# Performance work log

Measured on AMD Instinct MI355X. Metric: run time of the kernel, lower is better.

## Reference

```python
import jax, jax.numpy as jnp
import numpy as np

N_NODES = 20000
N_EDGES = 320000
EMB = 256
K_DIFF = 3
BN_EPS = 1e-5


def conv1d(x, w, b, stride):
    # x: [N, Cin, L], w: [Cout, Cin, K]
    y = jax.lax.conv_general_dilated(x, w, window_strides=(stride,), padding='VALID',
                                     dimension_numbers=('NCH', 'OIH', 'NCH'))
    return y + b[None, :, None]


def batchnorm_train(x, gamma, beta):
    # training-mode BatchNorm1d over (N, L) per channel, biased variance
    m = jnp.mean(x, axis=(0, 2), keepdims=True)
    v = jnp.var(x, axis=(0, 2), keepdims=True)
    return (x - m) * jax.lax.rsqrt(v + BN_EPS) * gamma[None, :, None] + beta[None, :, None]


def dconv(X, W, b, row, col, norm_out, norm_in, n):
    # Diffusion convolution (pytorch_geometric_temporal DConv), K hops,
    # forward (out-degree) and backward (in-degree) random walks.
    def prop(x, norm):
        msg = norm[:, None] * x[row]                    # [E, F] gather
        return jax.ops.segment_sum(msg, col, num_segments=n)  # scatter-add to targets

    K = W.shape[1]
    Tx_0 = X
    Tx_1 = X
    H = X @ W[0, 0] + X @ W[1, 0]
    if K > 1:
        Tx_1_o = prop(X, norm_out)
        Tx_1_i = prop(X, norm_in)
        H = H + Tx_1_o @ W[0, 1] + Tx_1_i @ W[1, 1]
    for k in range(2, K):
        Tx_2_o = 2.0 * prop(Tx_1_o, norm_out) - Tx_0
        Tx_2_i = 2.0 * prop(Tx_1_i, norm_in) - Tx_0
        H = H + Tx_2_o @ W[0, k] + Tx_2_i @ W[1, k]
        Tx_0, Tx_1_o, Tx_1_i = Tx_1, Tx_2_o, Tx_2_i
    return H + b


def setup_inputs() -> dict:
    key = jax.random.key(0)
    ks = jax.random.split(key, 16)
    d_in = 2 * EMB  # concat([X, H])
    inp = {
        'x': jax.random.normal(ks[0], (N_NODES, 1, 100), dtype=jnp.float32),
        'edge_index': jax.random.randint(ks[1], (2, N_EDGES), 0, N_NODES, dtype=jnp.int32),
        'hidden_state': jax.random.normal(ks[2], (N_NODES, EMB), dtype=jnp.float32),
        'conv1_w': jax.random.normal(ks[3], (32, 1, 10), dtype=jnp.float32) * 0.2,
        'conv1_b': jnp.zeros((32,), jnp.float32),
        'bn1_gamma': jnp.ones((32,), jnp.float32),
        'bn1_beta': jnp.zeros((32,), jnp.float32),
        'conv2_w': jax.random.normal(ks[4], (32, 32, 10), dtype=jnp.float32) * 0.05,
        'conv2_b': jnp.zeros((32,), jnp.float32),
        'bn2_gamma': jnp.ones((32,), jnp.float32),
        'bn2_beta': jnp.zeros((32,), jnp.float32),
        'W_z': jax.random.normal(ks[5], (2, K_DIFF, d_in, EMB), dtype=jnp.float32) * 0.05,
        'b_z': jnp.zeros((EMB,), jnp.float32),
        'W_r': jax.random.normal(ks[6], (2, K_DIFF, d_in, EMB), dtype=jnp.float32) * 0.05,
        'b_r': jnp.zeros((EMB,), jnp.float32),
        'W_h': jax.random.normal(ks[7], (2, K_DIFF, d_in, EMB), dtype=jnp.float32) * 0.05,
        'b_h': jnp.zeros((EMB,), jnp.float32),
    }
    return inp


def reference(x, edge_index, hidden_state, conv1_w, conv1_b, bn1_gamma, bn1_beta,
              conv2_w, conv2_b, bn2_gamma, bn2_beta, W_z, b_z, W_r, b_r, W_h, b_h):
    n = x.shape[0]
    # CNN embedding: conv -> relu -> bn, twice
    h = batchnorm_train(jax.nn.relu(conv1d(x, conv1_w, conv1_b, 3)), bn1_gamma, bn1_beta)
    h = batchnorm_train(jax.nn.relu(conv1d(h, conv2_w, conv2_b, 3)), bn2_gamma, bn2_beta)
    X = h.reshape(n, -1)  # [N, EMB]

    row, col = edge_index[0], edge_index[1]
    ones = jnp.ones((row.shape[0],), X.dtype)
    deg_out = jax.ops.segment_sum(ones, row, num_segments=n)
    deg_in = jax.ops.segment_sum(ones, col, num_segments=n)
    norm_out = (1.0 / deg_out)[row]
    norm_in = (1.0 / deg_in)[col]

    H0 = hidden_state
    XH = jnp.concatenate([X, H0], axis=1)
    Z = jax.nn.sigmoid(dconv(XH, W_z, b_z, row, col, norm_out, norm_in, n))
    R = jax.nn.sigmoid(dconv(XH, W_r, b_r, row, col, norm_out, norm_in, n))
    XRH = jnp.concatenate([X, R * H0], axis=1)
    H_tilde = jnp.tanh(dconv(XRH, W_h, b_h, row, col, norm_out, norm_in, n))
    H = Z * H0 + (1.0 - Z) * H_tilde
    return jax.nn.relu(H)
```

## Files before the change

### kernel.cpp

```cpp
#include <hip/hip_runtime.h>
#include <cstdint>
#include <cstddef>

#define NN 20000
#define NE 320000
#define SBUF 10240000

typedef float f32x4 __attribute__((ext_vector_type(4)));
typedef short s16x8 __attribute__((ext_vector_type(8)));
typedef unsigned short us;

__device__ __forceinline__ us f2bf(float x){
    unsigned u = __float_as_uint(x);
    unsigned r = (u + 0x7fffu + ((u >> 16) & 1u)) >> 16;
    return (us)r;
}
__device__ __forceinline__ float bf2f(us s){
    return __uint_as_float(((unsigned)s) << 16);
}

__device__ __forceinline__ void gl16(const void* g, void* l){
    __builtin_amdgcn_global_load_lds((const __attribute__((address_space(1))) unsigned int*)g,
                                     (__attribute__((address_space(3))) unsigned int*)l, 16, 0, 0);
}

__device__ __forceinline__ void upd8(uint4 v, float w, float* ao, float* ai){
    float f0=__uint_as_float(v.x<<16), f1=__uint_as_float(v.x&0xffff0000u);
    float f2=__uint_as_float(v.y<<16), f3=__uint_as_float(v.y&0xffff0000u);
    float f4=__uint_as_float(v.z<<16), f5=__uint_as_float(v.z&0xffff0000u);
    float f6=__uint_as_float(v.w<<16), f7=__uint_as_float(v.w&0xffff0000u);
    ao[0]=fmaf(w,f0,ao[0]); ao[1]=fmaf(w,f1,ao[1]); ao[2]=fmaf(w,f2,ao[2]); ao[3]=fmaf(w,f3,ao[3]);
    ao[4]=fmaf(w,f4,ao[4]); ao[5]=fmaf(w,f5,ao[5]); ao[6]=fmaf(w,f6,ao[6]); ao[7]=fmaf(w,f7,ao[7]);
    ai[0]+=f0; ai[1]+=f1; ai[2]+=f2; ai[3]+=f3; ai[4]+=f4; ai[5]+=f5; ai[6]+=f6; ai[7]+=f7;
}
__device__ __forceinline__ void updw(uint4 v, float w, float* a){
    float f0=__uint_as_float(v.x<<16), f1=__uint_as_float(v.x&0xffff0000u);
    float f2=__uint_as_float(v.y<<16), f3=__uint_as_float(v.y&0xffff0000u);
    float f4=__uint_as_float(v.z<<16), f5=__uint_as_float(v.z&0xffff0000u);
    float f6=__uint_as_float(v.w<<16), f7=__uint_as_float(v.w&0xffff0000u);
    a[0]=fmaf(w,f0,a[0]); a[1]=fmaf(w,f1,a[1]); a[2]=fmaf(w,f2,a[2]); a[3]=fmaf(w,f3,a[3]);
    a[4]=fmaf(w,f4,a[4]); a[5]=fmaf(w,f5,a[5]); a[6]=fmaf(w,f6,a[6]); a[7]=fmaf(w,f7,a[7]);
}
__device__ __forceinline__ uint4 pack8(const float* a){
    uint4 r;
    r.x=((unsigned)f2bf(a[1])<<16)|f2bf(a[0]);
    r.y=((unsigned)f2bf(a[3])<<16)|f2bf(a[2]);
    r.z=((unsigned)f2bf(a[5])<<16)|f2bf(a[4]);
    r.w=((unsigned)f2bf(a[7])<<16)|f2bf(a[6]);
    return r;
}
__device__ __forceinline__ uint4 pack8s(const float* a, float s){
    uint4 r;
    r.x=((unsigned)f2bf(s*a[1])<<16)|f2bf(s*a[0]);
    r.y=((unsigned)f2bf(s*a[3])<<16)|f2bf(s*a[2]);
    r.z=((unsigned)f2bf(s*a[5])<<16)|f2bf(s*a[4]);
    r.w=((unsigned)f2bf(s*a[7])<<16)|f2bf(s*a[6]);
    return r;
}


__global__ void k_zero(uint32_t* p, int n){
    int i = blockIdx.x*256 + threadIdx.x;
    if(i < n) p[i] = 0u;
}

__global__ void k_degree(const int* __restrict__ ei, int* degout, int* degin){
    int e = blockIdx.x*256 + threadIdx.x;
    if(e < NE){
        atomicAdd(&degout[ei[e]], 1);
        atomicAdd(&degin[ei[NE+e]], 1);
    }
}

__global__ void k_scan(const int* __restrict__ degin, int* __restrict__ coloff,
                       float* __restrict__ invdegin){
    __shared__ int part[1024];
    int t = threadIdx.x;
    int base = t*20;
    int s = 0;
    for(int k=0;k<20;k++){ int i = base+k; if(i < NN) s += degin[i]; }
    part[t] = s;
    __syncthreads();
    for(int off=1; off<1024; off<<=1){
        int v = (t>=off) ? part[t-off] : 0;
        __syncthreads();
        part[t] += v;
        __syncthreads();
    }
    int run = (t>0) ? part[t-1] : 0;
    for(int k=0;k<20;k++){
        int i = base+k;
        if(i < NN){
            int d = degin[i];
            coloff[i] = run;
            run += d;
            invdegin[i] = (d>0) ? (1.0f/(float)d) : 0.0f;
        }
    }
    if(t==1023) coloff[NN] = part[1023];
}

__global__ void k_csr(const int* __restrict__ ei, const int* __restrict__ degout,
                      const int* __restrict__ coloff, int* cnt, int2* __restrict__ ew){
    int e = blockIdx.x*256 + threadIdx.x;
    if(e < NE){
        int r = ei[e], c = ei[NE+e];
        int pos = coloff[c] + atomicAdd(&cnt[c], 1);
        int2 v; v.x = r; v.y = __float_as_int(1.0f/(float)degout[r]);
        ew[pos] = v;
    }
}


__global__ void k_conv1(const float* __restrict__ x, const float* __restrict__ w1,
                        const float* __restrict__ b1, us* __restrict__ y1T){
    __shared__ float w[320];
    __shared__ float bb[32];
    int t = threadIdx.x;
    for(int i=t;i<320;i+=256) w[i] = w1[i];
    if(t < 32) bb[t] = b1[t];
    __syncthreads();
    int gid = blockIdx.x*256 + t;
    int node = gid>>5, p = gid&31;
    us* yo = y1T + (size_t)node*1024 + p*32;
    if(p >= 31){
        uint4 z = {0,0,0,0};
        *(uint4*)yo = z; *(uint4*)(yo+8) = z;
        *(uint4*)(yo+16) = z; *(uint4*)(yo+24) = z;
        return;
    }
    const float* xr = x + node*100 + 3*p;
    float xv[10];
    #pragma unroll
    for(int k=0;k<10;k++) xv[k] = xr[k];
    float o[32];
    #pragma unroll
    for(int c=0;c<32;c++){
        float a = bb[c];
        #pragma unroll
        for(int k=0;k<10;k++) a = fmaf(w[c*10+k], xv[k], a);
        o[c] = fmaxf(a, 0.0f);
    }
    *(uint4*)yo      = pack8(o);
    *(uint4*)(yo+8)  = pack8(o+8);
    *(uint4*)(yo+16) = pack8(o+16);
    *(uint4*)(yo+24) = pack8(o+24);
}

__global__ void k_chanstats_T(const us* __restrict__ y, float* __restrict__ sq){
    int tid = blockIdx.x*256 + threadIdx.x;
    int slot = tid & 1023;
    int c = slot & 31;
    int node0 = tid >> 10;
    float s = 0.f, q = 0.f;
    for(int n=node0; n<NN; n+=64){
        float v = bf2f(y[(size_t)n*1024 + slot]);
        s += v; q = fmaf(v, v, q);
    }
    s += __shfl_xor(s, 32);
    q += __shfl_xor(q, 32);
    if((threadIdx.x & 63) < 32){
        atomicAdd(&sq[c], s);
        atomicAdd(&sq[32+c], q);
    }
}

template<int SLOTS, int PPC>
__global__ void k_chanstats_bf(const us* __restrict__ y, float* __restrict__ sq){
    int tid = blockIdx.x*blockDim.x + threadIdx.x;
    int slot = tid & (SLOTS-1);
    int node0 = tid / SLOTS;
    int nstride = (gridDim.x*blockDim.x) / SLOTS;
    int c = slot / PPC;
    float s = 0.f, q = 0.f;
    for(int n=node0; n<NN; n+=nstride){
        float v = bf2f(y[(size_t)n*SLOTS + slot]);
        s += v; q = fmaf(v, v, q);
    }
    #pragma unroll
    for(int m=PPC>>1; m>0; m>>=1){
        s += __shfl_xor(s, m);
        q += __shfl_xor(q, m);
    }
    if((threadIdx.x & (PPC-1)) == 0){
        atomicAdd(&sq[c], s);
        atomicAdd(&sq[32+c], q);
    }
}

__global__ void k_bnfin(const float* __restrict__ sq, const float* __restrict__ gamma,
                        const float* __restrict__ beta, float* __restrict__ scsh,
                        float inv_count){
    int c = threadIdx.x;
    if(c < 32){
        float m = sq[c]*inv_count;
        float v = sq[32+c]*inv_count - m*m;
        float sc = gamma[c]*rsqrtf(v + 1e-5f);
        scsh[c] = sc;
        scsh[32+c] = beta[c] - m*sc;
    }
}

__global__ void k_wfold(const float* __restrict__ w2, const float* __restrict__ scsh1,
                        us* __restrict__ Bf){
    int idx = blockIdx.x*256 + threadIdx.x;
    if(idx >= 10240) return;
    int kk = idx >> 10, c2 = (idx >> 5) & 31, c = idx & 31;
    Bf[idx] = f2bf(scsh1[c] * w2[c2*320 + c*10 + kk]);
}

__global__ void k_wbias(const float* __restrict__ w2, const float* __restrict__ scsh1,
                        const float* __restrict__ b2, float* __restrict__ biasc){
    int t = threadIdx.x;
    int c2 = t >> 3, part = t & 7;
    float s = 0.f;
    for(int i=part; i<320; i+=8)
        s += scsh1[32 + i/10] * w2[c2*320 + i];
    s += __shfl_xor(s,1); s += __shfl_xor(s,2); s += __shfl_xor(s,4);
    if(part == 0) biasc[c2] = b2[c2] + s;
}

__global__ void __launch_bounds__(256) k_conv2m(const us* __restrict__ y1T,
        const us* __restrict__ Bf, const float* __restrict__ biasc,
        us* __restrict__ Xpre){
    int t = threadIdx.x;
    int wv = t>>6, l = t&63;
    int l15 = l&15, g = l>>4;
    int r0 = blockIdx.x*64 + wv*16;
    int arow = r0 + l15;
    int an = arow>>3, ap = arow&7;
    const us* abase = y1T + (size_t)an*1024 + (3*ap)*32 + g*8;
    const us* bbase = Bf + (size_t)l15*32 + g*8;
    f32x4 acc0 = {}, acc1 = {};
    #pragma unroll
    for(int kk=0;kk<10;kk++){
        s16x8 af = *(const s16x8*)(abase + kk*32);
        s16x8 b0 = *(const s16x8*)(bbase + kk*1024);
        s16x8 b1 = *(const s16x8*)(bbase + kk*1024 + 512);
        acc0 = __builtin_amdgcn_mfma_f32_16x16x32_bf16(af, b0, acc0, 0, 0, 0);
        acc1 = __builtin_amdgcn_mfma_f32_16x16x32_bf16(af, b1, acc1, 0, 0, 0);
    }
    int base = r0 + g*4;
    int n = base>>3, p0 = base&7;
    #pragma unroll
    for(int nf=0;nf<2;nf++){
        int c2 = nf*16 + l15;
        float bb = biasc[c2];
        f32x4 a = nf ? acc1 : acc0;
        float v0 = fmaxf(a[0]+bb,0.f), v1 = fmaxf(a[1]+bb,0.f);
        float v2 = fmaxf(a[2]+bb,0.f), v3 = fmaxf(a[3]+bb,0.f);
        uint2 pk;
        pk.x = ((unsigned)f2bf(v1)<<16)|f2bf(v0);
        pk.y = ((unsigned)f2bf(v3)<<16)|f2bf(v2);
        *(uint2*)&Xpre[(size_t)n*256 + c2*8 + p0] = pk;
    }
}

__global__ void __launch_bounds__(256) k_prep(const us* __restrict__ Xpre,
        const float* __restrict__ scsh, const float* __restrict__ h0,
        us* __restrict__ XHp){
    int node = blockIdx.x*4 + (threadIdx.x>>6);
    if(node >= NN) return;
    int lane = threadIdx.x & 63;
    int half = lane>>5, g = lane&31;
    uint4 o;
    if(half == 0){
        uint4 v = *(const uint4*)(Xpre + (size_t)node*256 + g*8);
        float sc = scsh[g], sh = scsh[32+g];
        float y[8];
        y[0]=fmaf(sc,__uint_as_float(v.x<<16),sh); y[1]=fmaf(sc,__uint_as_float(v.x&0xffff0000u),sh);
        y[2]=fmaf(sc,__uint_as_float(v.y<<16),sh); y[3]=fmaf(sc,__uint_as_float(v.y&0xffff0000u),sh);
        y[4]=fmaf(sc,__uint_as_float(v.z<<16),sh); y[5]=fmaf(sc,__uint_as_float(v.z&0xffff0000u),sh);
        y[6]=fmaf(sc,__uint_as_float(v.w<<16),sh); y[7]=fmaf(sc,__uint_as_float(v.w&0xffff0000u),sh);
        o = pack8(y);
    }else{
        float4 a = *(const float4*)(h0 + (size_t)node*256 + g*8);
        float4 b = *(const float4*)(h0 + (size_t)node*256 + g*8 + 4);
        float y[8] = {a.x,a.y,a.z,a.w,b.x,b.y,b.z,b.w};
        o = pack8(y);
    }
    *(uint4*)(XHp + (size_t)node*512 + (size_t)g*16 + half*8) = o;
}


__device__ __forceinline__ float weff_val(const float* W, int term, size_t base){
    const size_t S = 512*256;
    if(term==0)      return W[0*S+base] + W[3*S+base] - W[2*S+base] - W[5*S+base];
    else if(term==1) return W[1*S+base];
    else if(term==2) return W[4*S+base];
    else if(term==3) return 2.0f*W[2*S+base];
    else             return 2.0f*W[5*S+base];
}

template<int NCOL>
__global__ void __launch_bounds__(256) k_wefft(const float* __restrict__ Wa,
        const float* __restrict__ Wb, us* __restrict__ Wt){
    __shared__ float tile[64*65];
    int bx = blockIdx.x;
    constexpr int CT = NCOL/64;
    int kb = bx / (CT*4);
    int rem = bx % (CT*4);
    int ct = rem >> 2, rt = rem & 3;
    int col0 = ct*64, rr0 = rt*64;
    const float* W = (col0 < 256) ? Wa : Wb;
    int jb = col0 & 255;
    int term = kb >> 1, half = kb & 1;
    int t = threadIdx.x;
    int j_l = t & 63, r4 = t >> 6;
    #pragma unroll
    for(int it=0; it<16; it++){
        int rr_l = it*4 + r4;
        int row = half*256 + rr0 + rr_l;
        size_t base = (size_t)row*256 + jb + j_l;
        tile[j_l*65 + rr_l] = weff_val(W, term, base);
    }
    __syncthreads();
    int rr_w = t & 63;
    #pragma unroll
    for(int it=0; it<16; it++){
        int col_l = it*4 + r4;
        Wt[(size_t)(col0+col_l)*2560 + kb*256 + rr0 + rr_w] = f2bf(tile[col_l*65 + rr_w]);
    }
}


__global__ void __launch_bounds__(256) k_prop1(const us* __restrict__ XHp,
        const int* __restrict__ coloff, const int2* __restrict__ ew,
        const float* __restrict__ invdeg, us* __restrict__ T1op, us* __restrict__ T1ip){
    int node = blockIdx.x*4 + (threadIdx.x>>6);
    if(node >= NN) return;
    int lane = threadIdx.x & 63;
    size_t lo = (size_t)(lane&31)*16 + (lane>>5)*8;
    int s = __builtin_amdgcn_readfirstlane(coloff[node]);
    int e = __builtin_amdgcn_readfirstlane(coloff[node+1]);
    float ao[8]={0,0,0,0,0,0,0,0}, ai[8]={0,0,0,0,0,0,0,0};
    int j = s;
    for(; j+7 < e; j += 8){
        int2 ed[8]; uint4 v[8];
        #pragma unroll
        for(int i=0;i<8;i++) ed[i] = ew[j+i];
        #pragma unroll
        for(int i=0;i<8;i++) v[i] = *(const uint4*)(XHp+(size_t)ed[i].x*512+lo);
        #pragma unroll
        for(int i=0;i<8;i++) upd8(v[i], __int_as_float(ed[i].y), ao, ai);
    }
    for(; j < e; j++){
        int2 ed = ew[j];
        uint4 v = *(const uint4*)(XHp+(size_t)ed.x*512+lo);
        upd8(v, __int_as_float(ed.y), ao, ai);
    }
    float wi = invdeg[node];
    *(uint4*)(T1op+(size_t)node*512+lo) = pack8(ao);
    *(uint4*)(T1ip+(size_t)node*512+lo) = pack8s(ai,wi);
}

__global__ void __launch_bounds__(256) k_prop2(const us* __restrict__ T1op,
        const us* __restrict__ T1ip,
        const int* __restrict__ coloff, const int2* __restrict__ ew,
        const float* __restrict__ invdeg, us* __restrict__ P2op, us* __restrict__ P2ip){
    int node = blockIdx.x*4 + (threadIdx.x>>6);
    if(node >= NN) return;
    int lane = threadIdx.x & 63;
    size_t lo = (size_t)(lane&31)*16 + (lane>>5)*8;
    int s = __builtin_amdgcn_readfirstlane(coloff[node]);
    int e = __builtin_amdgcn_readfirstlane(coloff[node+1]);
    float ao[8]={0,0,0,0,0,0,0,0}, ai[8]={0,0,0,0,0,0,0,0};
    int j = s;
    for(; j+3 < e; j += 4){
        int2 ed[4]; uint4 va[4], vb[4];
        #pragma unroll
        for(int i=0;i<4;i++) ed[i] = ew[j+i];
        #pragma unroll
        for(int i=0;i<4;i++){
            size_t o = (size_t)ed[i].x*512+lo;
            va[i] = *(const uint4*)(T1op+o);
            vb[i] = *(const uint4*)(T1ip+o);
        }
        #pragma unroll
        for(int i=0;i<4;i++){
            updw(va[i], __int_as_float(ed[i].y), ao);
            updw(vb[i], 1.0f, ai);
        }
    }
    for(; j < e; j++){
        int2 ed = ew[j];
        size_t o = (size_t)ed.x*512+lo;
        updw(*(const uint4*)(T1op+o), __int_as_float(ed.y), ao);
        updw(*(const uint4*)(T1ip+o), 1.0f, ai);
    }
    float wi = invdeg[node];
    *(uint4*)(P2op+(size_t)node*512+lo) = pack8(ao);
    *(uint4*)(P2ip+(size_t)node*512+lo) = pack8s(ai,wi);
}

__global__ void __launch_bounds__(256) k_propu(const us* __restrict__ Yin,
        const int* __restrict__ coloff, const int2* __restrict__ ew,
        const float* __restrict__ invdeg, us* __restrict__ Pout){
    int node = blockIdx.x*4 + (threadIdx.x>>6);
    if(node >= NN) return;
    int lane = threadIdx.x & 63;
    int half = lane>>5;
    size_t lo = (size_t)(lane&31)*16 + half*8;
    int s = __builtin_amdgcn_readfirstlane(coloff[node]);
    int e = __builtin_amdgcn_readfirstlane(coloff[node+1]);
    float a[8]={0,0,0,0,0,0,0,0};
    int j = s;
    for(; j+7 < e; j += 8){
        int2 ed[8]; uint4 v[8];
        #pragma unroll
        for(int i=0;i<8;i++) ed[i] = ew[j+i];
        #pragma unroll
        for(int i=0;i<8;i++) v[i] = *(const uint4*)(Yin+(size_t)ed[i].x*512+lo);
        #pragma unroll
        for(int i=0;i<8;i++) updw(v[i], half ? 1.0f : __int_as_float(ed[i].y), a);
    }
    for(; j < e; j++){
        int2 ed = ew[j];
        uint4 v = *(const uint4*)(Yin+(size_t)ed.x*512+lo);
        updw(v, half ? 1.0f : __int_as_float(ed.y), a);
    }
    float sc = half ? invdeg[node] : 1.0f;
    *(uint4*)(Pout+(size_t)node*512+lo) = pack8s(a,sc);
}


template<int MODE, int BNT>
__global__ void __launch_bounds__(256) k_gemm(const us* __restrict__ XG,
        const us* __restrict__ RG, const us* __restrict__ Wt,
        const float* __restrict__ bias0, const float* __restrict__ bias1,
        const float* __restrict__ h0, const float* __restrict__ Zin,
        float* __restrict__ out0, us* __restrict__ out1){
    constexpr int WN = BNT/32;
    constexpr int NB = BNT/64;
    __shared__ us As[3][4096];
    __shared__ us Bs[3][BNT*32];
    int t = threadIdx.x;
    int wid = t >> 6, lane = t & 63;
    int l15 = lane & 15, kg = lane >> 4;

    int bid = blockIdx.x;
    int xcd = bid & 7, sblk = bid >> 3;
    int cidx = sblk & 3, r = (sblk >> 2)*8 + xcd;
    if(r >= 157) return;
    int row0 = r*128, col0 = cidx*BNT;
    int rowbase = (wid >> 1)*64, colbase = (wid & 1)*(BNT/2);
    int swz = (l15 >> 1) & 3;

    int srA[2], sgA[2];
    size_t rowoffA[2];
    #pragma unroll
    for(int i=0;i<2;i++){
        int c = t + i*256;
        srA[i] = c >> 2;
        sgA[i] = (c & 3) ^ ((srA[i] >> 1) & 3);
        int gr = row0 + srA[i];
        gr = (gr < NN) ? gr : NN-1;
        rowoffA[i] = (size_t)gr*512 + (size_t)sgA[i]*16;
    }
    int srB[NB], sgB[NB];
    size_t coloffB[NB];
    #pragma unroll
    for(int i=0;i<NB;i++){
        int c = t + i*256;
        srB[i] = c >> 2;
        sgB[i] = (c & 3) ^ ((srB[i] >> 1) & 3);
        coloffB[i] = (size_t)(col0+srB[i])*2560 + (size_t)sgB[i]*8;
    }

    f32x4 acc[4][WN] = {};

    auto stage = [&](int buf, int s){
        int kb = s >> 3;
        int ktc = (s & 7) * 4;
        const us* Ap;
        if(MODE == 0){
            Ap = XG + (size_t)(kb >> 1) * SBUF + (size_t)(kb & 1) * 8;
        }else{
            if((kb & 1) == 0) Ap = XG + (size_t)(kb >> 1) * SBUF;
            else Ap = RG + (size_t)((kb + 1) >> 2) * SBUF + (size_t)(((kb + 1) >> 1) & 1) * 8;
        }
        #pragma unroll
        for(int i=0;i<2;i++)
            gl16(Ap + rowoffA[i] + (size_t)ktc*16, &As[buf][(t+i*256)*8]);
        const us* Wp = Wt + (size_t)kb*256 + (s & 7)*32;
        #pragma unroll
        for(int i=0;i<NB;i++)
            gl16(Wp + coloffB[i], &Bs[buf][(t+i*256)*8]);
    };

    stage(0, 0);
    stage(1, 1);
    int cur = 0;
    for(int step=0; step<80; ++step){
        if(step < 79){
            if(MODE == 0) asm volatile("s_waitcnt vmcnt(4)" ::: "memory");
            else          asm volatile("s_waitcnt vmcnt(3)" ::: "memory");
        }else{
            asm volatile("s_waitcnt vmcnt(0)" ::: "memory");
        }
        __builtin_amdgcn_s_barrier();
        __builtin_amdgcn_sched_barrier(0);
        s16x8 af[4], bfr[WN];
        #pragma unroll
        for(int i=0;i<4;i++){
            int row = rowbase + i*16 + l15;
            af[i] = *(const s16x8*)&As[cur][(row*4 + (kg ^ swz))*8];
        }
        #pragma unroll
        for(int n=0;n<WN;n++){
            int colr = colbase + n*16 + l15;
            bfr[n] = *(const s16x8*)&Bs[cur][(colr*4 + (kg ^ swz))*8];
        }
        if(step < 78){
            int nxt = cur + 2; if(nxt >= 3) nxt -= 3;
            stage(nxt, step+2);
        }
        __builtin_amdgcn_s_setprio(1);
        #pragma unroll
        for(int mi=0;mi<4;mi++){
            #pragma unroll
            for(int ni=0;ni<WN;ni++){
                acc[mi][ni] = __builtin_amdgcn_mfma_f32_16x16x32_bf16(
                    af[mi], bfr[ni], acc[mi][ni], 0, 0, 0);
            }
        }
        __builtin_amdgcn_s_setprio(0);
        cur = (cur == 2) ? 0 : cur + 1;
    }

    #pragma unroll
    for(int mi=0;mi<4;mi++){
        int gr0 = row0 + rowbase + mi*16 + kg*4;
        #pragma unroll
        for(int ni=0;ni<WN;ni++){
            int j = col0 + colbase + ni*16 + l15;
            #pragma unroll
            for(int rr=0;rr<4;rr++){
                int gr = gr0 + rr;
                if(gr < NN){
                    float a = acc[mi][ni][rr];
                    if(MODE == 0){
                        if(j < 256){
                            out0[(size_t)gr*256 + j] = 1.0f/(1.0f + expf(-(a + bias0[j])));
                        }else{
                            int jj = j - 256;
                            float rv = 1.0f/(1.0f + expf(-(a + bias1[jj])));
                            us v = f2bf(rv * h0[(size_t)gr*256 + jj]);
                            size_t base = (size_t)gr*512 + (size_t)(jj>>3)*16 + (jj&7);
                            out1[base] = v;
                            out1[base+8] = v;
                        }
                    }else{
                        float z = Zin[(size_t)gr*256 + j];
                        float ht = tanhf(a + bias0[j]);
                        float H = z*h0[(size_t)gr*256 + j] + (1.0f - z)*ht;
                        out0[(size_t)gr*256 + j] = fmaxf(H, 0.0f);
                    }
                }
            }
        }
    }
}


extern "C" void kernel_launch(void* const* d_in, const int* in_sizes, int n_in,
                              void* d_out, int out_size, void* d_ws, size_t ws_size,
                              hipStream_t stream){
    const float* x   = (const float*)d_in[0];
    const int*   ei  = (const int*)  d_in[1];
    const float* h0  = (const float*)d_in[2];
    const float* w1  = (const float*)d_in[3];
    const float* b1  = (const float*)d_in[4];
    const float* g1  = (const float*)d_in[5];
    const float* be1 = (const float*)d_in[6];
    const float* w2  = (const float*)d_in[7];
    const float* b2  = (const float*)d_in[8];
    const float* g2  = (const float*)d_in[9];
    const float* be2 = (const float*)d_in[10];
    const float* Wz  = (const float*)d_in[11];
    const float* bz  = (const float*)d_in[12];
    const float* Wr  = (const float*)d_in[13];
    const float* br  = (const float*)d_in[14];
    const float* Wh  = (const float*)d_in[15];
    const float* bh  = (const float*)d_in[16];
    float* out = (float*)d_out;
    float* wsf = (float*)d_ws;
    (void)in_sizes; (void)n_in; (void)out_size;

    const size_t O_DEGO=0, O_DEGI=20000, O_CNT=40000, O_BN=60000;
    const size_t O_COLOFF=60288, O_EW=80384, O_INVDEG=720384;
    const size_t O_WTZR=740480, O_WTH=1395840;
    const size_t O_XPRE=1723520;
    const size_t O_XG=4283520;
    const size_t O_RG=29883520;
    const size_t O_Z=45243520;
    const size_t O_BF=50363520;
    const size_t WS_NEED_BYTES = (size_t)50366080 * 4;
    if(ws_size < WS_NEED_BYTES) return;

    const size_t SW = 5120000;

    int* degout = (int*)(wsf + O_DEGO);
    int* degin  = (int*)(wsf + O_DEGI);
    int* cnt    = (int*)(wsf + O_CNT);
    float* bn   = wsf + O_BN;
    int* coloff = (int*)(wsf + O_COLOFF);
    int2* ew    = (int2*)(wsf + O_EW);
    float* invdeg = wsf + O_INVDEG;
    us* Wtzr = (us*)(wsf + O_WTZR);
    us* Wth  = (us*)(wsf + O_WTH);
    us* Xpre = (us*)(wsf + O_XPRE);
    us* XG   = (us*)(wsf + O_XG);
    us* RG   = (us*)(wsf + O_RG);
    us* XHp  = XG;
    us* T1op = (us*)(wsf + O_XG + SW);
    us* T1ip = (us*)(wsf + O_XG + 2*SW);
    us* P2op = (us*)(wsf + O_XG + 3*SW);
    us* P2ip = (us*)(wsf + O_XG + 4*SW);
    us* RHp  = RG;
    us* Q1p  = (us*)(wsf + O_RG + SW);
    us* Q2p  = (us*)(wsf + O_RG + 2*SW);
    float* Z = wsf + O_Z;
    us* Bf   = (us*)(wsf + O_BF);
    us* y1T  = T1op;

    k_zero<<<236,256,0,stream>>>((uint32_t*)(wsf + O_DEGO), 60256);
    k_degree<<<1250,256,0,stream>>>(ei, degout, degin);
    k_scan<<<1,1024,0,stream>>>(degin, coloff, invdeg);
    k_csr<<<1250,256,0,stream>>>(ei, degout, coloff, cnt, ew);

    k_conv1<<<2500,256,0,stream>>>(x, w1, b1, y1T);
    k_chanstats_T<<<256,256,0,stream>>>(y1T, bn+0);
    k_bnfin<<<1,32,0,stream>>>(bn+0, g1, be1, bn+64, 1.0f/620000.0f);
    k_wfold<<<40,256,0,stream>>>(w2, bn+64, Bf);
    k_wbias<<<1,256,0,stream>>>(w2, bn+64, b2, bn+256);
    k_conv2m<<<2500,256,0,stream>>>(y1T, Bf, bn+256, Xpre);
    k_chanstats_bf<256,8><<<64,256,0,stream>>>(Xpre, bn+128);
    k_bnfin<<<1,32,0,stream>>>(bn+128, g2, be2, bn+192, 1.0f/160000.0f);
    k_prep<<<5000,256,0,stream>>>(Xpre, bn+192, h0, XHp);

    k_wefft<512><<<320,256,0,stream>>>(Wz, Wr, Wtzr);
    k_wefft<256><<<160,256,0,stream>>>(Wh, Wh, Wth);

    k_prop1<<<5000,256,0,stream>>>(XHp, coloff, ew, invdeg, T1op, T1ip);
    k_prop2<<<5000,256,0,stream>>>(T1op, T1ip, coloff, ew, invdeg, P2op, P2ip);

    k_gemm<0,128><<<640,256,0,stream>>>(XG, RG, Wtzr, bz, br, h0, nullptr, Z, RHp);

    k_propu<<<5000,256,0,stream>>>(RHp, coloff, ew, invdeg, Q1p);
    k_propu<<<5000,256,0,stream>>>(Q1p, coloff, ew, invdeg, Q2p);

    k_gemm<1,64><<<640,256,0,stream>>>(XG, RG, Wth, bh, nullptr, h0, Z, out, nullptr);
}
```

Before: 734.7 us.

## Replace LDS triple-buffered GEMM pipeline with direct global-to-register MFMA loads

Removes the shared-memory staging (global_load_lds into a 3-stage ring with explicit vmcnt waits and barriers) from the gate GEMM kernels. Each wave now loads its A and B fragments directly from global memory into registers and feeds the MFMAs. This drops LDS traffic and block-level synchronisation, but loses data sharing between waves, so global and L2 traffic rises. It also loses explicit prefetching, leaving load latency to the compiler and to occupancy.

```diff
diff --git a/kernel.cpp b/kernel.cpp
--- a/kernel.cpp
+++ b/kernel.cpp
@@ -17,11 +17,6 @@
 }
 __device__ __forceinline__ float bf2f(us s){
     return __uint_as_float(((unsigned)s) << 16);
-}
-
-__device__ __forceinline__ void gl16(const void* g, void* l){
-    __builtin_amdgcn_global_load_lds((const __attribute__((address_space(1))) unsigned int*)g,
-                                     (__attribute__((address_space(3))) unsigned int*)l, 16, 0, 0);
 }
 
 __device__ __forceinline__ void upd8(uint4 v, float w, float* ao, float* ai){
@@ -424,54 +419,39 @@
 }
 
 
-template<int MODE, int BNT>
+template<int MODE, int WN>
 __global__ void __launch_bounds__(256) k_gemm(const us* __restrict__ XG,
         const us* __restrict__ RG, const us* __restrict__ Wt,
         const float* __restrict__ bias0, const float* __restrict__ bias1,
         const float* __restrict__ h0, const float* __restrict__ Zin,
         float* __restrict__ out0, us* __restrict__ out1){
-    constexpr int WN = BNT/32;
-    constexpr int NB = BNT/64;
-    __shared__ us As[3][4096];
-    __shared__ us Bs[3][BNT*32];
+    constexpr int BNT = WN*32;
     int t = threadIdx.x;
-    int wid = t >> 6, lane = t & 63;
-    int l15 = lane & 15, kg = lane >> 4;
+    int wv = t>>6, lane = t&63;
+    int l15 = lane&15, kg = lane>>4;
 
     int bid = blockIdx.x;
     int xcd = bid & 7, sblk = bid >> 3;
     int cidx = sblk & 3, r = (sblk >> 2)*8 + xcd;
     if(r >= 157) return;
-    int row0 = r*128, col0 = cidx*BNT;
-    int rowbase = (wid >> 1)*64, colbase = (wid & 1)*(BNT/2);
-    int swz = (l15 >> 1) & 3;
-
-    int srA[2], sgA[2];
-    size_t rowoffA[2];
-    #pragma unroll
-    for(int i=0;i<2;i++){
-        int c = t + i*256;
-        srA[i] = c >> 2;
-        sgA[i] = (c & 3) ^ ((srA[i] >> 1) & 3);
-        int gr = row0 + srA[i];
+    int row0 = r*128 + (wv>>1)*64;
+    int col0 = cidx*BNT + (wv&1)*(WN*16);
+
+    int aoff[4];
+    #pragma unroll
+    for(int i=0;i<4;i++){
+        int gr = row0 + i*16 + l15;
         gr = (gr < NN) ? gr : NN-1;
-        rowoffA[i] = (size_t)gr*512 + (size_t)sgA[i]*16;
-    }
-    int srB[NB], sgB[NB];
-    size_t coloffB[NB];
-    #pragma unroll
-    for(int i=0;i<NB;i++){
-        int c = t + i*256;
-        srB[i] = c >> 2;
-        sgB[i] = (c & 3) ^ ((srB[i] >> 1) & 3);
-        coloffB[i] = (size_t)(col0+srB[i])*2560 + (size_t)sgB[i]*8;
-    }
+        aoff[i] = gr*512 + kg*16;
+    }
+    int boff[WN];
+    #pragma unroll
+    for(int n=0;n<WN;n++)
+        boff[n] = (col0 + n*16 + l15)*2560 + kg*8;
 
     f32x4 acc[4][WN] = {};
 
-    auto stage = [&](int buf, int s){
-        int kb = s >> 3;
-        int ktc = (s & 7) * 4;
+    for(int kb=0; kb<10; ++kb){
         const us* Ap;
         if(MODE == 0){
             Ap = XG + (size_t)(kb >> 1) * SBUF + (size_t)(kb & 1) * 8;
@@ -479,61 +459,33 @@
             if((kb & 1) == 0) Ap = XG + (size_t)(kb >> 1) * SBUF;
             else Ap = RG + (size_t)((kb + 1) >> 2) * SBUF + (size_t)(((kb + 1) >> 1) & 1) * 8;
         }
-        #pragma unroll
-        for(int i=0;i<2;i++)
-            gl16(Ap + rowoffA[i] + (size_t)ktc*16, &As[buf][(t+i*256)*8]);
-        const us* Wp = Wt + (size_t)kb*256 + (s & 7)*32;
-        #pragma unroll
-        for(int i=0;i<NB;i++)
-            gl16(Wp + coloffB[i], &Bs[buf][(t+i*256)*8]);
-    };
-
-    stage(0, 0);
-    stage(1, 1);
-    int cur = 0;
-    for(int step=0; step<80; ++step){
-        if(step < 79){
-            if(MODE == 0) asm volatile("s_waitcnt vmcnt(4)" ::: "memory");
-            else          asm volatile("s_waitcnt vmcnt(3)" ::: "memory");
-        }else{
-            asm volatile("s_waitcnt vmcnt(0)" ::: "memory");
-        }
-        __builtin_amdgcn_s_barrier();
-        __builtin_amdgcn_sched_barrier(0);
-        s16x8 af[4], bfr[WN];
-        #pragma unroll
-        for(int i=0;i<4;i++){
-            int row = rowbase + i*16 + l15;
-            af[i] = *(const s16x8*)&As[cur][(row*4 + (kg ^ swz))*8];
-        }
-        #pragma unroll
-        for(int n=0;n<WN;n++){
-            int colr = colbase + n*16 + l15;
-            bfr[n] = *(const s16x8*)&Bs[cur][(colr*4 + (kg ^ swz))*8];
-        }
-        if(step < 78){
-            int nxt = cur + 2; if(nxt >= 3) nxt -= 3;
-            stage(nxt, step+2);
-        }
-        __builtin_amdgcn_s_setprio(1);
-        #pragma unroll
-        for(int mi=0;mi<4;mi++){
+        const us* Bp = Wt + kb*256;
+        #pragma unroll
+        for(int kt=0; kt<256; kt+=32){
+            s16x8 af[4], bf[WN];
             #pragma unroll
-            for(int ni=0;ni<WN;ni++){
-                acc[mi][ni] = __builtin_amdgcn_mfma_f32_16x16x32_bf16(
-                    af[mi], bfr[ni], acc[mi][ni], 0, 0, 0);
+            for(int i=0;i<4;i++)
+                af[i] = *(const s16x8*)(Ap + aoff[i] + kt*2);
+            #pragma unroll
+            for(int n=0;n<WN;n++)
+                bf[n] = *(const s16x8*)(Bp + boff[n] + kt);
+            #pragma unroll
+            for(int mi=0;mi<4;mi++){
+                #pragma unroll
+                for(int ni=0;ni<WN;ni++){
+                    acc[mi][ni] = __builtin_amdgcn_mfma_f32_16x16x32_bf16(
+                        af[mi], bf[ni], acc[mi][ni], 0, 0, 0);
+                }
             }
         }
-        __builtin_amdgcn_s_setprio(0);
-        cur = (cur == 2) ? 0 : cur + 1;
     }
 
     #pragma unroll
     for(int mi=0;mi<4;mi++){
-        int gr0 = row0 + rowbase + mi*16 + kg*4;
+        int gr0 = row0 + mi*16 + kg*4;
         #pragma unroll
         for(int ni=0;ni<WN;ni++){
-            int j = col0 + colbase + ni*16 + l15;
+            int j = col0 + ni*16 + l15;
             #pragma unroll
             for(int rr=0;rr<4;rr++){
                 int gr = gr0 + rr;
@@ -645,10 +597,10 @@
     k_prop1<<<5000,256,0,stream>>>(XHp, coloff, ew, invdeg, T1op, T1ip);
     k_prop2<<<5000,256,0,stream>>>(T1op, T1ip, coloff, ew, invdeg, P2op, P2ip);
 
-    k_gemm<0,128><<<640,256,0,stream>>>(XG, RG, Wtzr, bz, br, h0, nullptr, Z, RHp);
+    k_gemm<0,4><<<640,256,0,stream>>>(XG, RG, Wtzr, bz, br, h0, nullptr, Z, RHp);
 
     k_propu<<<5000,256,0,stream>>>(RHp, coloff, ew, invdeg, Q1p);
     k_propu<<<5000,256,0,stream>>>(Q1p, coloff, ew, invdeg, Q2p);
 
-    k_gemm<1,64><<<640,256,0,stream>>>(XG, RG, Wth, bh, nullptr, h0, Z, out, nullptr);
-}
+    k_gemm<1,2><<<640,256,0,stream>>>(XG, RG, Wth, bh, nullptr, h0, Z, out, nullptr);
+}
```

Result: slower. 999.3 us (+36.0%).

## Halve GEMM row tile, double-buffer LDS, store R*H compactly with dedicated propagation

Applied to the files above, without the earlier changes.

The GEMM kernels move from 128-row to 64-row tiles with twice the blocks, and from triple-buffered to double-buffered LDS with an extra barrier before restaging. The R*H output is now written once as a compact 256-wide bf16 row instead of duplicated into a 512-wide interleaved layout. A new k_propq1 kernel reads that compact layout, splitting edges across half-waves and combining the halves with shuffles. The aim is higher occupancy and less write and read traffic for R*H, at the cost of lower weight reuse per tile and less load/compute overlap.

```diff
diff --git a/kernel.cpp b/kernel.cpp
--- a/kernel.cpp
+++ b/kernel.cpp
@@ -393,6 +393,46 @@
     *(uint4*)(P2ip+(size_t)node*512+lo) = pack8s(ai,wi);
 }
 
+__global__ void __launch_bounds__(256) k_propq1(const us* __restrict__ RHb,
+        const int* __restrict__ coloff, const int2* __restrict__ ew,
+        const float* __restrict__ invdeg, us* __restrict__ Q1p){
+    int node = blockIdx.x*4 + (threadIdx.x>>6);
+    if(node >= NN) return;
+    int lane = threadIdx.x & 63;
+    int half = lane>>5, g = lane&31;
+    int s = __builtin_amdgcn_readfirstlane(coloff[node]);
+    int e = __builtin_amdgcn_readfirstlane(coloff[node+1]);
+    float ao[8]={0,0,0,0,0,0,0,0}, ai[8]={0,0,0,0,0,0,0,0};
+    int j = s;
+    for(; j+3 < e; j += 4){
+        int2 e0 = ew[j+half], e1 = ew[j+2+half];
+        uint4 v0 = *(const uint4*)(RHb+(size_t)e0.x*256+g*8);
+        uint4 v1 = *(const uint4*)(RHb+(size_t)e1.x*256+g*8);
+        upd8(v0, __int_as_float(e0.y), ao, ai);
+        upd8(v1, __int_as_float(e1.y), ao, ai);
+    }
+    for(; j+1 < e; j += 2){
+        int2 ed = ew[j+half];
+        uint4 v = *(const uint4*)(RHb+(size_t)ed.x*256+g*8);
+        upd8(v, __int_as_float(ed.y), ao, ai);
+    }
+    if(j < e && half == 0){
+        int2 ed = ew[j];
+        uint4 v = *(const uint4*)(RHb+(size_t)ed.x*256+g*8);
+        upd8(v, __int_as_float(ed.y), ao, ai);
+    }
+    #pragma unroll
+    for(int k=0;k<8;k++){
+        ao[k] += __shfl_xor(ao[k],32);
+        ai[k] += __shfl_xor(ai[k],32);
+    }
+    if(half == 0){
+        float wi = invdeg[node];
+        *(uint4*)(Q1p+(size_t)node*512+(size_t)g*16)   = pack8(ao);
+        *(uint4*)(Q1p+(size_t)node*512+(size_t)g*16+8) = pack8s(ai,wi);
+    }
+}
+
 __global__ void __launch_bounds__(256) k_propu(const us* __restrict__ Yin,
         const int* __restrict__ coloff, const int2* __restrict__ ew,
         const float* __restrict__ invdeg, us* __restrict__ Pout){
@@ -432,8 +472,9 @@
         float* __restrict__ out0, us* __restrict__ out1){
     constexpr int WN = BNT/32;
     constexpr int NB = BNT/64;
-    __shared__ us As[3][4096];
-    __shared__ us Bs[3][BNT*32];
+    constexpr int NVM = 1 + NB;
+    __shared__ us As[2][2048];
+    __shared__ us Bs[2][BNT*32];
     int t = threadIdx.x;
     int wid = t >> 6, lane = t & 63;
     int l15 = lane & 15, kg = lane >> 4;
@@ -441,22 +482,15 @@
     int bid = blockIdx.x;
     int xcd = bid & 7, sblk = bid >> 3;
     int cidx = sblk & 3, r = (sblk >> 2)*8 + xcd;
-    if(r >= 157) return;
-    int row0 = r*128, col0 = cidx*BNT;
-    int rowbase = (wid >> 1)*64, colbase = (wid & 1)*(BNT/2);
+    if(r >= 313) return;
+    int row0 = r*64, col0 = cidx*BNT;
+    int rowbase = (wid >> 1)*32, colbase = (wid & 1)*(BNT/2);
     int swz = (l15 >> 1) & 3;
 
-    int srA[2], sgA[2];
-    size_t rowoffA[2];
-    #pragma unroll
-    for(int i=0;i<2;i++){
-        int c = t + i*256;
-        srA[i] = c >> 2;
-        sgA[i] = (c & 3) ^ ((srA[i] >> 1) & 3);
-        int gr = row0 + srA[i];
-        gr = (gr < NN) ? gr : NN-1;
-        rowoffA[i] = (size_t)gr*512 + (size_t)sgA[i]*16;
-    }
+    int srA = t >> 2;
+    int sgA = (t & 3) ^ ((srA >> 1) & 3);
+    int grA = row0 + srA; grA = (grA < NN) ? grA : NN-1;
+    size_t rowoffA = (size_t)grA*512 + (size_t)sgA*16;
     int srB[NB], sgB[NB];
     size_t coloffB[NB];
     #pragma unroll
@@ -467,21 +501,23 @@
         coloffB[i] = (size_t)(col0+srB[i])*2560 + (size_t)sgB[i]*8;
     }
 
-    f32x4 acc[4][WN] = {};
+    f32x4 acc[2][WN] = {};
 
     auto stage = [&](int buf, int s){
         int kb = s >> 3;
         int ktc = (s & 7) * 4;
-        const us* Ap;
-        if(MODE == 0){
-            Ap = XG + (size_t)(kb >> 1) * SBUF + (size_t)(kb & 1) * 8;
+        if(MODE == 1 && kb == 1){
+            gl16(RG + (rowoffA >> 1) + (size_t)ktc*8, &As[buf][t*8]);
         }else{
-            if((kb & 1) == 0) Ap = XG + (size_t)(kb >> 1) * SBUF;
-            else Ap = RG + (size_t)((kb + 1) >> 2) * SBUF + (size_t)(((kb + 1) >> 1) & 1) * 8;
-        }
-        #pragma unroll
-        for(int i=0;i<2;i++)
-            gl16(Ap + rowoffA[i] + (size_t)ktc*16, &As[buf][(t+i*256)*8]);
+            const us* Ap;
+            if(MODE == 0){
+                Ap = XG + (size_t)(kb >> 1) * SBUF + (size_t)(kb & 1) * 8;
+            }else{
+                if((kb & 1) == 0) Ap = XG + (size_t)(kb >> 1) * SBUF;
+                else Ap = RG + (size_t)((kb + 1) >> 2) * SBUF + (size_t)(((kb + 1) >> 1) & 1) * 8;
+            }
+            gl16(Ap + rowoffA + (size_t)ktc*16, &As[buf][t*8]);
+        }
         const us* Wp = Wt + (size_t)kb*256 + (s & 7)*32;
         #pragma unroll
         for(int i=0;i<NB;i++)
@@ -490,19 +526,18 @@
 
     stage(0, 0);
     stage(1, 1);
-    int cur = 0;
     for(int step=0; step<80; ++step){
+        int cur = step & 1;
         if(step < 79){
-            if(MODE == 0) asm volatile("s_waitcnt vmcnt(4)" ::: "memory");
-            else          asm volatile("s_waitcnt vmcnt(3)" ::: "memory");
+            if(NVM == 3) asm volatile("s_waitcnt vmcnt(3)" ::: "memory");
+            else         asm volatile("s_waitcnt vmcnt(2)" ::: "memory");
         }else{
             asm volatile("s_waitcnt vmcnt(0)" ::: "memory");
         }
         __builtin_amdgcn_s_barrier();
-        __builtin_amdgcn_sched_barrier(0);
-        s16x8 af[4], bfr[WN];
-        #pragma unroll
-        for(int i=0;i<4;i++){
+        s16x8 af[2], bfr[WN];
+        #pragma unroll
+        for(int i=0;i<2;i++){
             int row = rowbase + i*16 + l15;
             af[i] = *(const s16x8*)&As[cur][(row*4 + (kg ^ swz))*8];
         }
@@ -511,13 +546,13 @@
             int colr = colbase + n*16 + l15;
             bfr[n] = *(const s16x8*)&Bs[cur][(colr*4 + (kg ^ swz))*8];
         }
-        if(step < 78){
-            int nxt = cur + 2; if(nxt >= 3) nxt -= 3;
-            stage(nxt, step+2);
-        }
+        asm volatile("s_waitcnt lgkmcnt(0)" ::: "memory");
+        __builtin_amdgcn_sched_barrier(0);
+        __builtin_amdgcn_s_barrier();
+        if(step < 78) stage(cur, step+2);
         __builtin_amdgcn_s_setprio(1);
         #pragma unroll
-        for(int mi=0;mi<4;mi++){
+        for(int mi=0;mi<2;mi++){
             #pragma unroll
             for(int ni=0;ni<WN;ni++){
                 acc[mi][ni] = __builtin_amdgcn_mfma_f32_16x16x32_bf16(
@@ -525,11 +560,10 @@
             }
         }
         __builtin_amdgcn_s_setprio(0);
-        cur = (cur == 2) ? 0 : cur + 1;
-    }
-
-    #pragma unroll
-    for(int mi=0;mi<4;mi++){
+    }
+
+    #pragma unroll
+    for(int mi=0;mi<2;mi++){
         int gr0 = row0 + rowbase + mi*16 + kg*4;
         #pragma unroll
         for(int ni=0;ni<WN;ni++){
@@ -545,10 +579,7 @@
                         }else{
                             int jj = j - 256;
                             float rv = 1.0f/(1.0f + expf(-(a + bias1[jj])));
-                            us v = f2bf(rv * h0[(size_t)gr*256 + jj]);
-                            size_t base = (size_t)gr*512 + (size_t)(jj>>3)*16 + (jj&7);
-                            out1[base] = v;
-                            out1[base+8] = v;
+                            out1[(size_t)gr*256 + jj] = f2bf(rv * h0[(size_t)gr*256 + jj]);
                         }
                     }else{
                         float z = Zin[(size_t)gr*256 + j];
@@ -617,7 +648,7 @@
     us* T1ip = (us*)(wsf + O_XG + 2*SW);
     us* P2op = (us*)(wsf + O_XG + 3*SW);
     us* P2ip = (us*)(wsf + O_XG + 4*SW);
-    us* RHp  = RG;
+    us* RHb  = RG;
     us* Q1p  = (us*)(wsf + O_RG + SW);
     us* Q2p  = (us*)(wsf + O_RG + 2*SW);
     float* Z = wsf + O_Z;
@@ -645,10 +676,10 @@
     k_prop1<<<5000,256,0,stream>>>(XHp, coloff, ew, invdeg, T1op, T1ip);
     k_prop2<<<5000,256,0,stream>>>(T1op, T1ip, coloff, ew, invdeg, P2op, P2ip);
 
-    k_gemm<0,128><<<640,256,0,stream>>>(XG, RG, Wtzr, bz, br, h0, nullptr, Z, RHp);
-
-    k_propu<<<5000,256,0,stream>>>(RHp, coloff, ew, invdeg, Q1p);
+    k_gemm<0,128><<<1280,256,0,stream>>>(XG, RG, Wtzr, bz, br, h0, nullptr, Z, RHb);
+
+    k_propq1<<<5000,256,0,stream>>>(RHb, coloff, ew, invdeg, Q1p);
     k_propu<<<5000,256,0,stream>>>(Q1p, coloff, ew, invdeg, Q2p);
 
-    k_gemm<1,64><<<640,256,0,stream>>>(XG, RG, Wth, bh, nullptr, h0, Z, out, nullptr);
-}
+    k_gemm<1,64><<<1280,256,0,stream>>>(XG, RG, Wth, bh, nullptr, h0, Z, out, nullptr);
+}
```

Result: faster. 720.1 us (-2.0%).
